# Kernel tuning notes

Measured on AMD Instinct MI355X. Metric: run time of the kernel, lower is better.

Reference implementation:

```python
import jax, jax.numpy as jnp
import numpy as np

N_NODES = 100000


def gcn_conv(x, edge_index, W, b, n_nodes):
    # PyG GCNConv: h = x @ W; add self-loops; symmetric normalization; aggregate to dst; + bias
    h = x @ W  # [N, out]
    loop = jnp.arange(n_nodes, dtype=edge_index.dtype)
    src = jnp.concatenate([edge_index[0], loop])
    dst = jnp.concatenate([edge_index[1], loop])
    ones = jnp.ones(src.shape[0], dtype=h.dtype)
    deg = jax.ops.segment_sum(ones, dst, num_segments=n_nodes)  # in-degree incl. self-loop
    dinv = jnp.where(deg > 0, jax.lax.rsqrt(deg), 0.0)
    norm = dinv[src] * dinv[dst]  # [E+N]
    msgs = h[src] * norm[:, None]  # gather + scale
    out = jax.ops.segment_sum(msgs, dst, num_segments=n_nodes)  # scatter-add
    return out + b


def setup_inputs() -> dict:
    key = jax.random.key(0)
    k1, k2, k3, k4 = jax.random.split(key, 4)
    x = jax.random.normal(k1, (N_NODES, 256), dtype=jnp.float32)
    edge_index = jax.random.randint(k2, (2, 3200000), 0, N_NODES, dtype=jnp.int64)
    W1 = jax.random.normal(k3, (256, 64), dtype=jnp.float32) * (1.0 / np.sqrt(256))
    b1 = jnp.zeros((64,), dtype=jnp.float32)
    W2 = jax.random.normal(k4, (64, 40), dtype=jnp.float32) * (1.0 / np.sqrt(64))
    b2 = jnp.zeros((40,), dtype=jnp.float32)
    return {"x": x, "edge_index": edge_index, "W1": W1, "b1": b1, "W2": W2, "b2": b2}


def reference(x, edge_index, W1, b1, W2, b2):
    n = x.shape[0]
    h = gcn_conv(x, edge_index, W1, b1, n)
    h = jax.nn.relu(h)
    h = gcn_conv(h, edge_index, W2, b2, n)
    return jax.nn.log_softmax(h, axis=1)
```

## Files before the change

kernel.cpp:

```cpp
#include <hip/hip_runtime.h>
#include <hip/hip_bf16.h>
#include <math.h>

static constexpr int NN    = 100000;
static constexpr int BSH   = 9;
static constexpr int NBUCK = (NN + 511) >> 9;
static constexpr int EPB   = 8192;
static constexpr int CAP   = 24576;

typedef __attribute__((ext_vector_type(8))) short short8;
typedef __attribute__((ext_vector_type(4))) float f32x4;
typedef __attribute__((ext_vector_type(2))) float f32x2;

#if defined(__has_builtin)
#  if __has_builtin(__builtin_amdgcn_cvt_pk_f32_fp8) && __has_builtin(__builtin_amdgcn_cvt_pk_fp8_f32)
#    define USE_HW_FP8 1
#  endif
#endif
#ifndef USE_HW_FP8
#  define USE_HW_FP8 0
#endif

__device__ __forceinline__ short f2bf(float f) {
    __hip_bfloat16 h = __float2bfloat16(f);
    return __builtin_bit_cast(short, h);
}

__device__ __forceinline__ float fp8_dec_sw(unsigned b) {
    unsigned u = ((b & 0x80u) << 24) | ((b & 0x7Fu) << 20);
    return __builtin_bit_cast(float, u) * 0x1p120f;
}
__device__ __forceinline__ unsigned fp8_enc_sw(float f) {
    unsigned u = __builtin_bit_cast(unsigned, f * 0x1p-120f);
    unsigned s = (u >> 24) & 0x80u;
    unsigned mag = u & 0x7FFFFFFFu;
    unsigned t = mag + 0x7FFFFu + ((mag >> 20) & 1u);
    unsigned r = t >> 20;
    if (r > 0x7Eu) r = 0x7Eu;
    return s | r;
}

template<bool HI>
__device__ __forceinline__ f32x2 dec2w(unsigned u) {
#if USE_HW_FP8
    return __builtin_amdgcn_cvt_pk_f32_fp8(u, HI);
#else
    unsigned w = HI ? (u >> 16) : u;
    f32x2 r;
    r.x = fp8_dec_sw(w & 0xFFu);
    r.y = fp8_dec_sw((w >> 8) & 0xFFu);
    return r;
#endif
}
__device__ __forceinline__ unsigned enc2(float a, float b) {
#if USE_HW_FP8
    return (unsigned)__builtin_amdgcn_cvt_pk_fp8_f32(a, b, 0, false);
#else
    return fp8_enc_sw(a) | (fp8_enc_sw(b) << 8);
#endif
}

__device__ __forceinline__ void acc8(f32x2* a, uint2 u) {
    a[0] += dec2w<false>(u.x);
    a[1] += dec2w<true>(u.x);
    a[2] += dec2w<false>(u.y);
    a[3] += dec2w<true>(u.y);
}
__device__ __forceinline__ void acc8s(f32x2* a, uint2 u, float ds) {
    f32x2 w = {ds, ds};
    a[0] = dec2w<false>(u.x) * w + a[0];
    a[1] = dec2w<true>(u.x)  * w + a[1];
    a[2] = dec2w<false>(u.y) * w + a[2];
    a[3] = dec2w<true>(u.y)  * w + a[3];
}

__device__ __forceinline__ long long ldidx(const void* __restrict__ p, long long i, int is64) {
    if (is64) return ((const long long* __restrict__)p)[i];
    return (long long)((const int* __restrict__)p)[i];
}

template<int K, int NCOLS, int KT, int NT>
__device__ __forceinline__ void packB_dev(const float* __restrict__ W,
                                          short* __restrict__ P, int t) {
    if (t >= KT * NT * 64) return;
    int kt = t / (NT * 64);
    int nt = (t / 64) % NT;
    int l  = t & 63;
    int g  = l >> 4;
#pragma unroll
    for (int e = 0; e < 8; ++e) {
        int k   = kt * 32 + g * 8 + e;
        int col = nt * 16 + (l & 15);
        float v = (col < NCOLS) ? W[k * NCOLS + col] : 0.0f;
        P[t * 8 + e] = f2bf(v);
    }
}

__global__ void __launch_bounds__(256)
k_init(const unsigned int* __restrict__ e32, int* __restrict__ flag,
       int* __restrict__ gcur,
       const float* __restrict__ W1, short* __restrict__ pB1,
       const float* __restrict__ W2, short* __restrict__ pB2) {
    int blk = blockIdx.x, tid = threadIdx.x;
    if (blk == 0) {
        if (tid < NBUCK) gcur[tid] = 0;
        __shared__ int any_nz;
        if (tid == 0) any_nz = 0;
        __syncthreads();
        unsigned int nz = 0;
        for (int w = 1 + 2 * tid; w < 4096; w += 512)
            nz |= e32[w];
        if (nz) atomicOr(&any_nz, 1);
        __syncthreads();
        if (tid == 0) *flag = (any_nz == 0) ? 1 : 0;
    } else if (blk <= 8) {
        packB_dev<256, 64, 8, 4>(W1, pB1, (blk - 1) * 256 + tid);
    } else {
        packB_dev<64, 40, 2, 3>(W2, pB2, (blk - 9) * 256 + tid);
    }
}

__global__ void __launch_bounds__(1024)
k_build_gemm1(const void* __restrict__ eidx, const int* __restrict__ flag, long long E,
              int nsblk, int ngblk, int* __restrict__ gcur, unsigned* __restrict__ ebuf,
              const float* __restrict__ X, const short* __restrict__ pB1,
              unsigned char* __restrict__ H, int n) {
    int bid = (int)blockIdx.x;
    int mn = nsblk < ngblk ? nsblk : ngblk;
    int role, idx;
    if (bid < 2 * mn) { role = bid & 1; idx = bid >> 1; }
    else {
        int rem = bid - 2 * mn;
        role = (nsblk > ngblk) ? 0 : 1;
        idx = mn + rem;
    }
    if (role == 0) {
        __shared__ int h[NBUCK];
        for (int b = threadIdx.x; b < NBUCK; b += 1024) h[b] = 0;
        __syncthreads();
        int is64 = *flag;
        long long base = (long long)idx * EPB;
        long long end  = base + EPB < E ? base + EPB : E;
        unsigned sv[8], dv[8];
        bool ok[8];
#pragma unroll
        for (int k = 0; k < 8; ++k) {
            long long e = base + (long long)k * 1024 + threadIdx.x;
            ok[k] = (e < end);
            if (ok[k]) {
                sv[k] = (unsigned)ldidx(eidx, e, is64);
                dv[k] = (unsigned)ldidx(eidx, E + e, is64);
                atomicAdd(&h[dv[k] >> BSH], 1);
            }
        }
        __syncthreads();
        for (int b = threadIdx.x; b < NBUCK; b += 1024)
            h[b] = atomicAdd(&gcur[b], h[b]);
        __syncthreads();
#pragma unroll
        for (int k = 0; k < 8; ++k) {
            if (ok[k]) {
                int bk = dv[k] >> BSH;
                int pos = atomicAdd(&h[bk], 1);
                ebuf[(long long)bk * CAP + pos] = sv[k] | ((dv[k] & 511u) << 17);
            }
        }
    } else {
        __shared__ alignas(16) short sW[8 * 4 * 512];
        __shared__ alignas(16) short sX[64 * 264];
        short8* dst = (short8*)sW;
        const short8* src = (const short8*)pB1;
        int tid = threadIdx.x;
        for (int i = tid; i < 2048; i += 1024) dst[i] = src[i];

        int wave = tid >> 6, lane = tid & 63;
        int g   = lane >> 4;
        int wig = wave >> 2;
        int nt  = wave & 3;

        int lr = tid >> 4;
        int c0 = (tid & 15) * 16;

        for (int s = 0; s < 4; ++s) {
            int grow = idx * 256 + s * 64 + lr;
            short8 lo, hi;
            if (grow < n) {
                const float* xr = X + (long long)grow * 256 + c0;
                float4 u0 = *(const float4*)(xr);
                float4 u1 = *(const float4*)(xr + 4);
                float4 u2 = *(const float4*)(xr + 8);
                float4 u3 = *(const float4*)(xr + 12);
                lo[0] = f2bf(u0.x); lo[1] = f2bf(u0.y); lo[2] = f2bf(u0.z); lo[3] = f2bf(u0.w);
                lo[4] = f2bf(u1.x); lo[5] = f2bf(u1.y); lo[6] = f2bf(u1.z); lo[7] = f2bf(u1.w);
                hi[0] = f2bf(u2.x); hi[1] = f2bf(u2.y); hi[2] = f2bf(u2.z); hi[3] = f2bf(u2.w);
                hi[4] = f2bf(u3.x); hi[5] = f2bf(u3.y); hi[6] = f2bf(u3.z); hi[7] = f2bf(u3.w);
            } else {
                lo = (short8){0,0,0,0,0,0,0,0};
                hi = lo;
            }
            __syncthreads();
            *(short8*)&sX[lr * 264 + c0]     = lo;
            *(short8*)&sX[lr * 264 + c0 + 8] = hi;
            __syncthreads();

            f32x4 acc = (f32x4){0.f, 0.f, 0.f, 0.f};
            const short* arow_p = &sX[(wig * 16 + (lane & 15)) * 264];
#pragma unroll
            for (int kt = 0; kt < 8; ++kt) {
                short8 a = *(const short8*)(arow_p + kt * 32 + g * 8);
                short8 bfr = dst[(kt * 4 + nt) * 64 + lane];
                acc = __builtin_amdgcn_mfma_f32_16x16x32_bf16(a, bfr, acc, 0, 0, 0);
            }
            int c = nt * 16 + (lane & 15);
            int orow_base = idx * 256 + s * 64 + wig * 16 + g * 4;
#pragma unroll
            for (int r = 0; r < 4; ++r) {
                int orow = orow_base + r;
                if (orow < n)
                    H[(long long)orow * 64 + c] =
                        (unsigned char)(enc2(acc[r], 0.0f) & 0xFFu);
            }
        }
    }
}

__global__ void __launch_bounds__(1024)
k_bucket_csr(const unsigned* __restrict__ ebuf, const int* __restrict__ gcnt,
             int* __restrict__ rowst, float* __restrict__ dinv,
             int* __restrict__ csr, int n) {
    __shared__ int cnt[512];
    __shared__ int cursor[512];
    __shared__ int woff[8];
    __shared__ int bs_sh;
    int b = blockIdx.x;
    int t = threadIdx.x;
    int cb = gcnt[b];
    long long rbase = (long long)b * CAP;
    if (t == 0) bs_sh = 0;
    if (t < 512) cnt[t] = 0;
    __syncthreads();
    if (t < b) atomicAdd(&bs_sh, gcnt[t]);
    unsigned ev[24];
#pragma unroll
    for (int k = 0; k < 24; ++k) {
        int i = t + k * 1024;
        if (i < cb) {
            ev[k] = ebuf[rbase + i];
            atomicAdd(&cnt[ev[k] >> 17], 1);
        }
    }
    __syncthreads();
    int bs = bs_sh;
    if (b == NBUCK - 1 && t == 0) rowst[n] = bs + cb;
    int v = 0, ps = 0;
    if (t < 512) {
        v = cnt[t];
        ps = v;
        int lane = t & 63;
#pragma unroll
        for (int off = 1; off < 64; off <<= 1) {
            int up = __shfl_up(ps, off);
            if (lane >= off) ps += up;
        }
        if (lane == 63) woff[t >> 6] = ps;
    }
    __syncthreads();
    if (t == 0) {
        int run = 0;
#pragma unroll
        for (int i = 0; i < 8; ++i) { int x = woff[i]; woff[i] = run; run += x; }
    }
    __syncthreads();
    if (t < 512) {
        int incl  = ps + woff[t >> 6];
        int start = bs + incl - v;
        int gnode = (b << BSH) + t;
        if (gnode < n) {
            rowst[gnode] = start;
            dinv[gnode]  = rsqrtf((float)(v + 1));
        }
        cursor[t] = start;
    }
    __syncthreads();
#pragma unroll
    for (int k = 0; k < 24; ++k) {
        int i = t + k * 1024;
        if (i < cb) {
            int pos = atomicAdd(&cursor[ev[k] >> 17], 1);
            csr[pos] = (int)(ev[k] & 0x1FFFFu);
        }
    }
}

template<int K, int NCOLS, int KT, int NT, bool ABF16>
__global__ void __launch_bounds__(256)
k_mfma_gemm(const void* __restrict__ Xv, const short* __restrict__ packedB,
            const float* __restrict__ dinv, unsigned char* __restrict__ H, int n) {
    __shared__ alignas(16) short sW[KT * NT * 512];
    short8* dst = (short8*)sW;
    const short8* src = (const short8*)packedB;
    constexpr int TOT8 = KT * NT * 64;
    for (int i = threadIdx.x; i < TOT8; i += 256) dst[i] = src[i];
    __syncthreads();

    int wave = threadIdx.x >> 6, lane = threadIdx.x & 63;
    int g = lane >> 4;
    int arow = blockIdx.x * 64 + wave * 16 + (lane & 15);

    f32x4 acc[NT];
#pragma unroll
    for (int nt = 0; nt < NT; ++nt) acc[nt] = (f32x4){0.f, 0.f, 0.f, 0.f};

#pragma unroll
    for (int kt = 0; kt < KT; ++kt) {
        short8 a;
        if (arow < n) {
            int k0 = kt * 32 + g * 8;
            if (ABF16) {
                const short* xr = (const short*)Xv + (long long)arow * K;
                a = *(const short8*)(xr + k0);
            } else {
                const float* xr = (const float*)Xv + (long long)arow * K;
                float4 u = *(const float4*)(xr + k0);
                float4 v = *(const float4*)(xr + k0 + 4);
                a[0] = f2bf(u.x); a[1] = f2bf(u.y); a[2] = f2bf(u.z); a[3] = f2bf(u.w);
                a[4] = f2bf(v.x); a[5] = f2bf(v.y); a[6] = f2bf(v.z); a[7] = f2bf(v.w);
            }
        } else {
            a = (short8){0, 0, 0, 0, 0, 0, 0, 0};
        }
#pragma unroll
        for (int nt = 0; nt < NT; ++nt) {
            short8 bfr = dst[(kt * NT + nt) * 64 + lane];
            acc[nt] = __builtin_amdgcn_mfma_f32_16x16x32_bf16(a, bfr, acc[nt], 0, 0, 0);
        }
    }

    int c = lane & 15;
    int orow_base = blockIdx.x * 64 + wave * 16 + g * 4;
#pragma unroll
    for (int r = 0; r < 4; ++r) {
        int orow = orow_base + r;
        if (orow < n) {
            float di = dinv[orow];
            float v[NT];
#pragma unroll
            for (int nt = 0; nt < NT; ++nt) v[nt] = acc[nt][r] * di;
            unsigned char* hp = H + (long long)orow * NCOLS;
#pragma unroll
            for (int p = 0; p < NT; p += 2) {
                unsigned wrd = enc2(v[p], (p + 1 < NT) ? v[p + 1] : 0.0f);
                int col0 = p * 16 + c;
                if (col0 < NCOLS) hp[col0] = (unsigned char)(wrd & 0xFFu);
                if (p + 1 < NT) {
                    int col1 = col0 + 16;
                    if (col1 < NCOLS) hp[col1] = (unsigned char)((wrd >> 8) & 0xFFu);
                }
            }
        }
    }
}

__global__ void __launch_bounds__(256)
k_gather_relu(const int* __restrict__ rowst, const int* __restrict__ csr,
              const unsigned char* __restrict__ h1s, const float* __restrict__ dinv,
              const float* __restrict__ b, unsigned short* __restrict__ out, int n) {
    long long gid = (long long)blockIdx.x * blockDim.x + threadIdx.x;
    int node = (int)(gid >> 4);
    int sub  = (int)(gid & 15);
    int eg   = sub >> 3;
    int fe   = sub & 7;
    if (node >= n) return;
    int jb = rowst[node], je = rowst[node + 1];
    unsigned feoff = (unsigned)fe << 3;

    f32x2 a0[4], a1[4], a2[4], a3[4];
#pragma unroll
    for (int q = 0; q < 4; ++q) {
        a0[q] = (f32x2){0.f, 0.f}; a1[q] = (f32x2){0.f, 0.f};
        a2[q] = (f32x2){0.f, 0.f}; a3[q] = (f32x2){0.f, 0.f};
    }

    int j = jb + eg;
    for (; j + 6 < je; j += 8) {
        int s0 = csr[j], s1 = csr[j + 2], s2 = csr[j + 4], s3 = csr[j + 6];
        float ds0 = dinv[s0], ds1 = dinv[s1], ds2 = dinv[s2], ds3 = dinv[s3];
        uint2 u0 = *(const uint2*)(h1s + (((unsigned)s0 << 6) + feoff));
        uint2 u1 = *(const uint2*)(h1s + (((unsigned)s1 << 6) + feoff));
        uint2 u2 = *(const uint2*)(h1s + (((unsigned)s2 << 6) + feoff));
        uint2 u3 = *(const uint2*)(h1s + (((unsigned)s3 << 6) + feoff));
        acc8s(a0, u0, ds0);
        acc8s(a1, u1, ds1);
        acc8s(a2, u2, ds2);
        acc8s(a3, u3, ds3);
    }
    for (; j < je; j += 2) {
        int s0 = csr[j];
        float ds0 = dinv[s0];
        uint2 u0 = *(const uint2*)(h1s + (((unsigned)s0 << 6) + feoff));
        acc8s(a0, u0, ds0);
    }
#pragma unroll
    for (int q = 0; q < 4; ++q) a0[q] += (a1[q] + a2[q]) + a3[q];

#pragma unroll
    for (int q = 0; q < 4; ++q) {
        a0[q].x += __shfl_xor(a0[q].x, 8);
        a0[q].y += __shfl_xor(a0[q].y, 8);
    }

    if (eg == 0) {
        float dn = dinv[node];
        uint2 self = *(const uint2*)(h1s + (((unsigned)node << 6) + feoff));
        acc8s(a0, self, dn);
        unsigned short r[8];
#pragma unroll
        for (int q = 0; q < 4; ++q) {
            float v0 = fmaxf(a0[q].x * dn + b[8 * fe + 2 * q],     0.0f);
            float v1 = fmaxf(a0[q].y * dn + b[8 * fe + 2 * q + 1], 0.0f);
            r[2 * q]     = (unsigned short)f2bf(v0);
            r[2 * q + 1] = (unsigned short)f2bf(v1);
        }
        uint4 pk;
        pk.x = (unsigned)r[0] | ((unsigned)r[1] << 16);
        pk.y = (unsigned)r[2] | ((unsigned)r[3] << 16);
        pk.z = (unsigned)r[4] | ((unsigned)r[5] << 16);
        pk.w = (unsigned)r[6] | ((unsigned)r[7] << 16);
        ((uint4*)(out + (long long)node * 64))[fe] = pk;
    }
}

__global__ void __launch_bounds__(256)
k_gather_lsm(const int* __restrict__ rowst, const int* __restrict__ csr,
             const unsigned char* __restrict__ h2s, const float* __restrict__ dinv,
             const float* __restrict__ b, float* __restrict__ out, int n) {
    long long gid = (long long)blockIdx.x * blockDim.x + threadIdx.x;
    int node = (int)(gid >> 4);
    int sub  = (int)(gid & 15);
    int eg   = sub >> 3;
    int fe   = sub & 7;
    if (node >= n) return;
    bool act = (fe < 5);
    int jb = rowst[node], je = rowst[node + 1];
    unsigned feoff = (unsigned)fe << 3;

    f32x2 a0[4], a1[4], a2[4], a3[4];
#pragma unroll
    for (int q = 0; q < 4; ++q) {
        a0[q] = (f32x2){0.f, 0.f}; a1[q] = (f32x2){0.f, 0.f};
        a2[q] = (f32x2){0.f, 0.f}; a3[q] = (f32x2){0.f, 0.f};
    }

    int j = jb + eg;
    for (; j + 6 < je; j += 8) {
        int s0 = csr[j], s1 = csr[j + 2], s2 = csr[j + 4], s3 = csr[j + 6];
        if (act) {
            uint2 u0 = *(const uint2*)(h2s + ((unsigned)s0 * 40u + feoff));
            uint2 u1 = *(const uint2*)(h2s + ((unsigned)s1 * 40u + feoff));
            uint2 u2 = *(const uint2*)(h2s + ((unsigned)s2 * 40u + feoff));
            uint2 u3 = *(const uint2*)(h2s + ((unsigned)s3 * 40u + feoff));
            acc8(a0, u0);
            acc8(a1, u1);
            acc8(a2, u2);
            acc8(a3, u3);
        }
    }
    for (; j < je; j += 2) {
        int s0 = csr[j];
        if (act) {
            uint2 u0 = *(const uint2*)(h2s + ((unsigned)s0 * 40u + feoff));
            acc8(a0, u0);
        }
    }
#pragma unroll
    for (int q = 0; q < 4; ++q) a0[q] += (a1[q] + a2[q]) + a3[q];

#pragma unroll
    for (int q = 0; q < 4; ++q) {
        a0[q].x += __shfl_xor(a0[q].x, 8);
        a0[q].y += __shfl_xor(a0[q].y, 8);
    }

    float va[8];
    float mloc = -INFINITY;
    if (act) {
        uint2 self = *(const uint2*)(h2s + ((unsigned)node * 40u + feoff));
        acc8(a0, self);
        float di = dinv[node];
#pragma unroll
        for (int q = 0; q < 4; ++q) {
            va[2 * q]     = a0[q].x * di + b[8 * fe + 2 * q];
            va[2 * q + 1] = a0[q].y * di + b[8 * fe + 2 * q + 1];
            mloc = fmaxf(mloc, fmaxf(va[2 * q], va[2 * q + 1]));
        }
    }
    float m = mloc;
    m = fmaxf(m, __shfl_xor(m, 1));
    m = fmaxf(m, __shfl_xor(m, 2));
    m = fmaxf(m, __shfl_xor(m, 4));
    m = fmaxf(m, __shfl_xor(m, 8));
    float ex = 0.0f;
    if (act && eg == 0) {
#pragma unroll
        for (int k = 0; k < 8; ++k) ex += __expf(va[k] - m);
    }
    ex += __shfl_xor(ex, 1);
    ex += __shfl_xor(ex, 2);
    ex += __shfl_xor(ex, 4);
    ex += __shfl_xor(ex, 8);
    float lse = __logf(ex);
    if (act && eg == 0) {
        float4 r0 = make_float4(va[0] - m - lse, va[1] - m - lse,
                                va[2] - m - lse, va[3] - m - lse);
        float4 r1 = make_float4(va[4] - m - lse, va[5] - m - lse,
                                va[6] - m - lse, va[7] - m - lse);
        *(float4*)(out + (long long)node * 40 + 8 * fe)     = r0;
        *(float4*)(out + (long long)node * 40 + 8 * fe + 4) = r1;
    }
}

extern "C" void kernel_launch(void* const* d_in, const int* in_sizes, int n_in,
                              void* d_out, int out_size, void* d_ws, size_t ws_size,
                              hipStream_t stream) {
    const float* x  = (const float*)d_in[0];
    const void*  ei = d_in[1];
    const float* W1 = (const float*)d_in[2];
    const float* b1 = (const float*)d_in[3];
    const float* W2 = (const float*)d_in[4];
    const float* b2 = (const float*)d_in[5];
    float* out = (float*)d_out;

    const long long E = (long long)in_sizes[1] / 2;
    const int nsblk = (int)((E + EPB - 1) / EPB);
    const int ngblk = (NN + 255) / 256;

    char* w = (char*)d_ws;
    auto alloc = [&](size_t bytes) -> void* {
        void* p = (void*)w;
        w += (bytes + 255) & ~(size_t)255;
        return p;
    };
    int*      flag    = (int*)     alloc(4);
    int*      gcur    = (int*)     alloc((size_t)NBUCK * 4);
    int*      rowst   = (int*)     alloc(((size_t)NN + 1) * 4);
    float*    dinv    = (float*)   alloc((size_t)NN * 4);
    short*    pB1     = (short*)   alloc((size_t)8 * 4 * 64 * 8 * 2);
    short*    pB2     = (short*)   alloc((size_t)2 * 3 * 64 * 8 * 2);
    int*      csr     = (int*)     alloc((size_t)E * 4);
    unsigned* ebuf    = (unsigned*)alloc((size_t)NBUCK * CAP * 4);
    unsigned char* h1s = (unsigned char*)alloc((size_t)NN * 64);
    unsigned short* agg1 = (unsigned short*)alloc((size_t)NN * 64 * 2);
    unsigned char* h2s = h1s;

    const int B = 256;
    auto cdiv = [](long long a, long long b) { return (int)((a + b - 1) / b); };

    k_init<<<11, B, 0, stream>>>((const unsigned int*)ei, flag, gcur, W1, pB1, W2, pB2);

    k_build_gemm1<<<nsblk + ngblk, 1024, 0, stream>>>(ei, flag, E, nsblk, ngblk,
                                                      gcur, ebuf, x, pB1, h1s, NN);

    k_bucket_csr<<<NBUCK, 1024, 0, stream>>>(ebuf, gcur, rowst, dinv, csr, NN);

    k_gather_relu<<<cdiv((long long)NN * 16, B), B, 0, stream>>>(rowst, csr, h1s, dinv, b1, agg1, NN);

    k_mfma_gemm<64, 40, 2, 3, true><<<cdiv(NN, 64), B, 0, stream>>>(agg1, pB2, dinv, h2s, NN);

    k_gather_lsm<<<cdiv((long long)NN * 16, B), B, 0, stream>>>(rowst, csr, h2s, dinv, b2, out, NN);
}
```

Measured before the change: 174.8 us.

## Fuse layer-1 gather/ReLU with layer-2 MFMA GEMM via shared memory

Merges the layer-1 aggregation kernel and the second GEMM into one kernel. Each 256-thread block aggregates 16 nodes, writes the bf16 ReLU rows to LDS, then three waves run MFMA against the packed W2 and write the scaled fp8 h2. This removes the round trip of the 100000x64 bf16 intermediate through global memory and one kernel launch. In exchange it adds a block-wide barrier after the irregular gather, idles one wave during the GEMM, and reads W2 fragments from global memory instead of LDS. h2s now gets its own buffer instead of aliasing h1s, which is required because other blocks are still reading h1s.

```diff
diff --git a/kernel.cpp b/kernel.cpp
--- a/kernel.cpp
+++ b/kernel.cpp
@@ -292,87 +292,19 @@
     }
 }
 
-template<int K, int NCOLS, int KT, int NT, bool ABF16>
 __global__ void __launch_bounds__(256)
-k_mfma_gemm(const void* __restrict__ Xv, const short* __restrict__ packedB,
-            const float* __restrict__ dinv, unsigned char* __restrict__ H, int n) {
-    __shared__ alignas(16) short sW[KT * NT * 512];
-    short8* dst = (short8*)sW;
-    const short8* src = (const short8*)packedB;
-    constexpr int TOT8 = KT * NT * 64;
-    for (int i = threadIdx.x; i < TOT8; i += 256) dst[i] = src[i];
-    __syncthreads();
-
-    int wave = threadIdx.x >> 6, lane = threadIdx.x & 63;
-    int g = lane >> 4;
-    int arow = blockIdx.x * 64 + wave * 16 + (lane & 15);
-
-    f32x4 acc[NT];
-#pragma unroll
-    for (int nt = 0; nt < NT; ++nt) acc[nt] = (f32x4){0.f, 0.f, 0.f, 0.f};
-
-#pragma unroll
-    for (int kt = 0; kt < KT; ++kt) {
-        short8 a;
-        if (arow < n) {
-            int k0 = kt * 32 + g * 8;
-            if (ABF16) {
-                const short* xr = (const short*)Xv + (long long)arow * K;
-                a = *(const short8*)(xr + k0);
-            } else {
-                const float* xr = (const float*)Xv + (long long)arow * K;
-                float4 u = *(const float4*)(xr + k0);
-                float4 v = *(const float4*)(xr + k0 + 4);
-                a[0] = f2bf(u.x); a[1] = f2bf(u.y); a[2] = f2bf(u.z); a[3] = f2bf(u.w);
-                a[4] = f2bf(v.x); a[5] = f2bf(v.y); a[6] = f2bf(v.z); a[7] = f2bf(v.w);
-            }
-        } else {
-            a = (short8){0, 0, 0, 0, 0, 0, 0, 0};
-        }
-#pragma unroll
-        for (int nt = 0; nt < NT; ++nt) {
-            short8 bfr = dst[(kt * NT + nt) * 64 + lane];
-            acc[nt] = __builtin_amdgcn_mfma_f32_16x16x32_bf16(a, bfr, acc[nt], 0, 0, 0);
-        }
-    }
-
-    int c = lane & 15;
-    int orow_base = blockIdx.x * 64 + wave * 16 + g * 4;
-#pragma unroll
-    for (int r = 0; r < 4; ++r) {
-        int orow = orow_base + r;
-        if (orow < n) {
-            float di = dinv[orow];
-            float v[NT];
-#pragma unroll
-            for (int nt = 0; nt < NT; ++nt) v[nt] = acc[nt][r] * di;
-            unsigned char* hp = H + (long long)orow * NCOLS;
-#pragma unroll
-            for (int p = 0; p < NT; p += 2) {
-                unsigned wrd = enc2(v[p], (p + 1 < NT) ? v[p + 1] : 0.0f);
-                int col0 = p * 16 + c;
-                if (col0 < NCOLS) hp[col0] = (unsigned char)(wrd & 0xFFu);
-                if (p + 1 < NT) {
-                    int col1 = col0 + 16;
-                    if (col1 < NCOLS) hp[col1] = (unsigned char)((wrd >> 8) & 0xFFu);
-                }
-            }
-        }
-    }
-}
-
-__global__ void __launch_bounds__(256)
-k_gather_relu(const int* __restrict__ rowst, const int* __restrict__ csr,
-              const unsigned char* __restrict__ h1s, const float* __restrict__ dinv,
-              const float* __restrict__ b, unsigned short* __restrict__ out, int n) {
-    long long gid = (long long)blockIdx.x * blockDim.x + threadIdx.x;
-    int node = (int)(gid >> 4);
-    int sub  = (int)(gid & 15);
+k_gather_relu_gemm2(const int* __restrict__ rowst, const int* __restrict__ csr,
+                    const unsigned char* __restrict__ h1s, const float* __restrict__ dinv,
+                    const float* __restrict__ b, const short* __restrict__ pB2,
+                    unsigned char* __restrict__ h2s, int n) {
+    __shared__ alignas(16) short sA[16 * 72];
+    int tid  = threadIdx.x;
+    int nl   = tid >> 4;
+    int node = blockIdx.x * 16 + nl;
+    int sub  = tid & 15;
     int eg   = sub >> 3;
     int fe   = sub & 7;
-    if (node >= n) return;
-    int jb = rowst[node], je = rowst[node + 1];
-    unsigned feoff = (unsigned)fe << 3;
+    bool nok = (node < n);
 
     f32x2 a0[4], a1[4], a2[4], a3[4];
 #pragma unroll
@@ -380,25 +312,28 @@
         a0[q] = (f32x2){0.f, 0.f}; a1[q] = (f32x2){0.f, 0.f};
         a2[q] = (f32x2){0.f, 0.f}; a3[q] = (f32x2){0.f, 0.f};
     }
-
-    int j = jb + eg;
-    for (; j + 6 < je; j += 8) {
-        int s0 = csr[j], s1 = csr[j + 2], s2 = csr[j + 4], s3 = csr[j + 6];
-        float ds0 = dinv[s0], ds1 = dinv[s1], ds2 = dinv[s2], ds3 = dinv[s3];
-        uint2 u0 = *(const uint2*)(h1s + (((unsigned)s0 << 6) + feoff));
-        uint2 u1 = *(const uint2*)(h1s + (((unsigned)s1 << 6) + feoff));
-        uint2 u2 = *(const uint2*)(h1s + (((unsigned)s2 << 6) + feoff));
-        uint2 u3 = *(const uint2*)(h1s + (((unsigned)s3 << 6) + feoff));
-        acc8s(a0, u0, ds0);
-        acc8s(a1, u1, ds1);
-        acc8s(a2, u2, ds2);
-        acc8s(a3, u3, ds3);
-    }
-    for (; j < je; j += 2) {
-        int s0 = csr[j];
-        float ds0 = dinv[s0];
-        uint2 u0 = *(const uint2*)(h1s + (((unsigned)s0 << 6) + feoff));
-        acc8s(a0, u0, ds0);
+    if (nok) {
+        int jb = rowst[node], je = rowst[node + 1];
+        unsigned feoff = (unsigned)fe << 3;
+        int j = jb + eg;
+        for (; j + 6 < je; j += 8) {
+            int s0 = csr[j], s1 = csr[j + 2], s2 = csr[j + 4], s3 = csr[j + 6];
+            float ds0 = dinv[s0], ds1 = dinv[s1], ds2 = dinv[s2], ds3 = dinv[s3];
+            uint2 u0 = *(const uint2*)(h1s + (((unsigned)s0 << 6) + feoff));
+            uint2 u1 = *(const uint2*)(h1s + (((unsigned)s1 << 6) + feoff));
+            uint2 u2 = *(const uint2*)(h1s + (((unsigned)s2 << 6) + feoff));
+            uint2 u3 = *(const uint2*)(h1s + (((unsigned)s3 << 6) + feoff));
+            acc8s(a0, u0, ds0);
+            acc8s(a1, u1, ds1);
+            acc8s(a2, u2, ds2);
+            acc8s(a3, u3, ds3);
+        }
+        for (; j < je; j += 2) {
+            int s0 = csr[j];
+            float ds0 = dinv[s0];
+            uint2 u0 = *(const uint2*)(h1s + (((unsigned)s0 << 6) + feoff));
+            acc8s(a0, u0, ds0);
+        }
     }
 #pragma unroll
     for (int q = 0; q < 4; ++q) a0[q] += (a1[q] + a2[q]) + a3[q];
@@ -409,24 +344,48 @@
         a0[q].y += __shfl_xor(a0[q].y, 8);
     }
 
-    if (eg == 0) {
+    if (eg == 0 && nok) {
         float dn = dinv[node];
+        unsigned feoff = (unsigned)fe << 3;
         uint2 self = *(const uint2*)(h1s + (((unsigned)node << 6) + feoff));
         acc8s(a0, self, dn);
-        unsigned short r[8];
+        short* rowp = &sA[nl * 72 + fe * 8];
 #pragma unroll
         for (int q = 0; q < 4; ++q) {
             float v0 = fmaxf(a0[q].x * dn + b[8 * fe + 2 * q],     0.0f);
             float v1 = fmaxf(a0[q].y * dn + b[8 * fe + 2 * q + 1], 0.0f);
-            r[2 * q]     = (unsigned short)f2bf(v0);
-            r[2 * q + 1] = (unsigned short)f2bf(v1);
-        }
-        uint4 pk;
-        pk.x = (unsigned)r[0] | ((unsigned)r[1] << 16);
-        pk.y = (unsigned)r[2] | ((unsigned)r[3] << 16);
-        pk.z = (unsigned)r[4] | ((unsigned)r[5] << 16);
-        pk.w = (unsigned)r[6] | ((unsigned)r[7] << 16);
-        ((uint4*)(out + (long long)node * 64))[fe] = pk;
+            rowp[2 * q]     = f2bf(v0);
+            rowp[2 * q + 1] = f2bf(v1);
+        }
+    } else if (eg == 0) {
+        short* rowp = &sA[nl * 72 + fe * 8];
+#pragma unroll
+        for (int k = 0; k < 8; ++k) rowp[k] = 0;
+    }
+    __syncthreads();
+
+    int wave = tid >> 6, lane = tid & 63;
+    if (wave < 3) {
+        int g = lane >> 4;
+        f32x4 acc = (f32x4){0.f, 0.f, 0.f, 0.f};
+#pragma unroll
+        for (int kt = 0; kt < 2; ++kt) {
+            short8 a = *(const short8*)&sA[(lane & 15) * 72 + kt * 32 + g * 8];
+            short8 bfr = ((const short8*)pB2)[(kt * 3 + wave) * 64 + lane];
+            acc = __builtin_amdgcn_mfma_f32_16x16x32_bf16(a, bfr, acc, 0, 0, 0);
+        }
+        int c = wave * 16 + (lane & 15);
+        if (c < 40) {
+#pragma unroll
+            for (int r = 0; r < 4; ++r) {
+                int onode = blockIdx.x * 16 + g * 4 + r;
+                if (onode < n) {
+                    float di = dinv[onode];
+                    h2s[(long long)onode * 40 + c] =
+                        (unsigned char)(enc2(acc[r] * di, 0.0f) & 0xFFu);
+                }
+            }
+        }
     }
 }
 
@@ -549,8 +508,7 @@
     int*      csr     = (int*)     alloc((size_t)E * 4);
     unsigned* ebuf    = (unsigned*)alloc((size_t)NBUCK * CAP * 4);
     unsigned char* h1s = (unsigned char*)alloc((size_t)NN * 64);
-    unsigned short* agg1 = (unsigned short*)alloc((size_t)NN * 64 * 2);
-    unsigned char* h2s = h1s;
+    unsigned char* h2s = (unsigned char*)alloc((size_t)NN * 40);
 
     const int B = 256;
     auto cdiv = [](long long a, long long b) { return (int)((a + b - 1) / b); };
@@ -562,9 +520,8 @@
 
     k_bucket_csr<<<NBUCK, 1024, 0, stream>>>(ebuf, gcur, rowst, dinv, csr, NN);
 
-    k_gather_relu<<<cdiv((long long)NN * 16, B), B, 0, stream>>>(rowst, csr, h1s, dinv, b1, agg1, NN);
-
-    k_mfma_gemm<64, 40, 2, 3, true><<<cdiv(NN, 64), B, 0, stream>>>(agg1, pB2, dinv, h2s, NN);
+    k_gather_relu_gemm2<<<cdiv((long long)NN * 16, B), B, 0, stream>>>(
+        rowst, csr, h1s, dinv, b1, pB2, h2s, NN);
 
     k_gather_lsm<<<cdiv((long long)NN * 16, B), B, 0, stream>>>(rowst, csr, h2s, dinv, b2, out, NN);
 }
```

Result: faster. 170.2 us (-2.6%).
